# Optimization experiments

Measured on AMD Instinct MI355X. Metric: run time of the kernel, lower is better.

## Reference

```python
import jax, jax.numpy as jnp
import numpy as np

B, S, D = 1, 2048, 512
H, KH, DH = 8, 2, 64
G = H // KH            # grouped queries per kv head
CBS = SBS = 32         # compress / selection block size (equal)
NSEL = 8               # num selected blocks
WIN = 128              # sliding window size
NC = S // CBS          # num compressed blocks
NF = S // SBS          # num fine blocks (S divisible by SBS)
CDIM = CBS * DH


def setup_inputs():
    key = jax.random.key(0)
    ks = jax.random.split(key, 12)
    r = lambda k, shape, s=0.02: jax.random.normal(k, shape, dtype=jnp.float32) * s
    return {
        "inp": jax.random.normal(ks[0], (B, S, D), dtype=jnp.float32),
        "norm_w": jnp.ones((D,), jnp.float32),
        "w_qkv": r(ks[1], (D, H * DH + 2 * KH * DH)),
        "mem_kv": r(ks[2], (2, KH, 1, DH)),
        "k_pos": r(ks[3], (KH, CBS, DH)),
        "v_pos": r(ks[4], (KH, CBS, DH)),
        "kc_w1": r(ks[5], (CDIM, CDIM)), "kc_b1": jnp.zeros((CDIM,), jnp.float32),
        "kc_w2": r(ks[6], (CDIM, DH)), "kc_b2": jnp.zeros((DH,), jnp.float32),
        "vc_w1": r(ks[7], (CDIM, CDIM)), "vc_b1": jnp.zeros((CDIM,), jnp.float32),
        "vc_w2": r(ks[8], (CDIM, DH)), "vc_b2": jnp.zeros((DH,), jnp.float32),
        "comb_w": r(ks[9], (D, 3 * H)),
        "comb_b": jnp.tile(jnp.array([-2.0, -2.0, 2.0], jnp.float32), H),
        "out_w": r(ks[10], (H * DH, D)),
    }


def _rope(x):  # x: [b, h, n, d]; interleaved rotary (rotary-embedding-torch style)
    d, n = x.shape[-1], x.shape[-2]
    inv = 1.0 / (10000.0 ** (jnp.arange(0, d, 2, dtype=jnp.float32) / d))
    fr = jnp.arange(n, dtype=jnp.float32)[:, None] * inv[None, :]  # [n, d/2]
    fr = jnp.repeat(fr, 2, axis=-1)                                 # [n, d]
    cos, sin = jnp.cos(fr), jnp.sin(fr)
    xp = x.reshape(*x.shape[:-1], d // 2, 2)
    xr = jnp.stack((-xp[..., 1], xp[..., 0]), axis=-1).reshape(x.shape)
    return x * cos + xr * sin


def _mlp(x, w1, b1, w2, b2):
    return jax.nn.relu(x @ w1 + b1) @ w2 + b2


def _forward(inp, norm_w, w_qkv, mem_kv, k_pos, v_pos, kc_w1, kc_b1, kc_w2, kc_b2,
             vc_w1, vc_b1, vc_w2, vc_b2, comb_w, comb_b, out_w):
    scale = DH ** -0.5
    NEG = -jnp.finfo(jnp.float32).max

    # RMSNorm
    x = inp * jax.lax.rsqrt(jnp.mean(inp * inp, -1, keepdims=True)
                            + jnp.finfo(jnp.float32).eps) * norm_w

    qkv = x @ w_qkv
    q, k, v = jnp.split(qkv, [H * DH, H * DH + KH * DH], axis=-1)
    q = q.reshape(B, S, H, DH).transpose(0, 2, 1, 3)    # b h n d
    k = k.reshape(B, S, KH, DH).transpose(0, 2, 1, 3)   # b kh n d
    v = v.reshape(B, S, KH, DH).transpose(0, 2, 1, 3)

    # --- 1. compressed attention (unrotated q/k) ---
    kb = k.reshape(B, KH, NC, CBS, DH) + k_pos[None, :, None]
    vb = v.reshape(B, KH, NC, CBS, DH) + v_pos[None, :, None]
    ck = _mlp(kb.reshape(B, KH, NC, CDIM), kc_w1, kc_b1, kc_w2, kc_b2)  # b kh nc d
    cv = _mlp(vb.reshape(B, KH, NC, CDIM), vc_w1, vc_b1, vc_w2, vc_b2)
    ck = jnp.concatenate((jnp.broadcast_to(mem_kv[0][None], (B, KH, 1, DH)), ck), axis=2)
    cv = jnp.concatenate((jnp.broadcast_to(mem_kv[1][None], (B, KH, 1, DH)), cv), axis=2)

    ck_pos = jnp.concatenate((jnp.array([-1]), (jnp.arange(NC) + 1) * CBS - 1))
    cmask = ck_pos[None, :] < jnp.arange(S)[:, None]     # [S, 1+NC]

    qg = q.reshape(B, KH, G, S, DH)
    csim = jnp.einsum('bhgid,bhjd->bhgij', qg, ck) * scale
    csim = jnp.where(cmask, csim, NEG)
    cattn = jax.nn.softmax(csim, axis=-1)
    c_out = jnp.einsum('bhgij,bhjd->bhgid', cattn, cv)   # b kh g n d

    # --- importance scores -> top-k block selection (shared across grouped queries) ---
    imp = csim[..., 1:].mean(axis=2)                     # b kh n nc
    imp = jnp.pad(imp, ((0, 0), (0, 0), (0, 0), (1, 0)), constant_values=-1e3)
    imp = jax.nn.softmax(imp, axis=-1)[..., 1:]
    sel_val, sel_idx = jax.lax.top_k(imp, NSEL)          # b kh n sel

    # --- rotary for fine + sliding branches ---
    qr, kr = _rope(q), _rope(k)

    # --- 2. fine (selected-block) attention ---
    own = jnp.broadcast_to((jnp.arange(S) // SBS)[None, None, :, None], (B, KH, S, 1))
    sel_idx = jnp.concatenate((sel_idx, own), axis=-1)   # b kh n (sel+1), own block appended

    bmask = jnp.broadcast_to((sel_val > 1e-10)[..., None], (B, KH, S, NSEL, SBS))
    tri = jnp.tril(jnp.ones((SBS, SBS), bool))
    diag = jnp.broadcast_to(jnp.tile(tri, (NF, 1))[None, None, :, None, :], (B, KH, S, 1, SBS))
    fmask = jnp.concatenate((bmask, diag), axis=-2).reshape(B, KH, 1, S, (NSEL + 1) * SBS)

    kfb = kr.reshape(B, KH, NF, SBS, DH)
    vfb = v.reshape(B, KH, NF, SBS, DH)
    gidx = sel_idx[..., None, None]                      # b kh n sel1 1 1
    fk = jnp.take_along_axis(kfb[:, :, None], gidx, axis=3).reshape(B, KH, S, (NSEL + 1) * SBS, DH)
    fv = jnp.take_along_axis(vfb[:, :, None], gidx, axis=3).reshape(B, KH, S, (NSEL + 1) * SBS, DH)

    fqg = qr.reshape(B, KH, G, S, DH)
    fsim = jnp.einsum('bhgid,bhijd->bhgij', fqg, fk) * scale
    fsim = jnp.where(fmask, fsim, NEG)
    fattn = jax.nn.softmax(fsim, axis=-1)
    f_out = jnp.einsum('bhgij,bhijd->bhgid', fattn, fv)  # b kh g n d

    diff = jnp.arange(S)[:, None] - jnp.arange(S)[None, :]
    smask = (diff >= 0) & (diff <= WIN)
    ssim = jnp.einsum('bhgid,bhjd->bhgij', fqg, kr) * scale
    ssim = jnp.where(smask, ssim, NEG)
    sattn = jax.nn.softmax(ssim, axis=-1)
    s_out = jnp.einsum('bhgij,bhjd->bhgid', sattn, v)    # b kh g n d

    # --- learned gating combine over [compressed, fine, sliding] ---
    gates = jax.nn.sigmoid(x @ comb_w + comb_b).reshape(B, S, H, 3)
    gates = gates.transpose(0, 2, 1, 3).reshape(B, KH, G, S, 3)
    out = gates[..., 0:1] * c_out + gates[..., 1:2] * f_out + gates[..., 2:3] * s_out
    out = out.reshape(B, H, S, DH).transpose(0, 2, 1, 3).reshape(B, S, H * DH)
    return out @ out_w


def reference(inp, norm_w, w_qkv, mem_kv, k_pos, v_pos, kc_w1, kc_b1, kc_w2, kc_b2,
              vc_w1, vc_b1, vc_w2, vc_b2, comb_w, comb_b, out_w):
    return _forward(inp, norm_w, w_qkv, mem_kv, k_pos, v_pos, kc_w1, kc_b1, kc_w2, kc_b2,
                    vc_w1, vc_b1, vc_w2, vc_b2, comb_w, comb_b, out_w)
```

## Files before the change

kernel.cpp:

```cpp
#include <hip/hip_runtime.h>
#include <hip/hip_bf16.h>
#include <math.h>

#define S 2048
#define D 512
#define H 8
#define KH 2
#define DH 64
#define G 4
#define CBS 32
#define NSEL 8
#define WIN 128
#define NC 64
#define CDIM 2048

typedef __attribute__((ext_vector_type(8))) short bf16x8_t;
typedef __attribute__((ext_vector_type(4))) float f32x4_t;
typedef __attribute__((ext_vector_type(2))) _Float16 half2v;

static __device__ __forceinline__ unsigned short f2bf(float f) {
    union { float f; unsigned int u; } v; v.f = f;
    unsigned int r = (v.u + 0x7FFFu + ((v.u >> 16) & 1u)) >> 16;
    return (unsigned short)r;
}
static __device__ __forceinline__ float bf2f(unsigned short h) {
    union { unsigned int u; float f; } v; v.u = ((unsigned int)h) << 16;
    return v.f;
}
static __device__ __forceinline__ float bflo(unsigned int u) {
    union { unsigned int u; float f; } v; v.u = u << 16; return v.f;
}
static __device__ __forceinline__ float bfhi(unsigned int u) {
    union { unsigned int u; float f; } v; v.u = u & 0xffff0000u; return v.f;
}
static __device__ __forceinline__ unsigned short f2h(float f) {
    union { _Float16 h; unsigned short s; } v; v.h = (_Float16)f; return v.s;
}
static __device__ __forceinline__ float h2f(unsigned short u) {
    union { unsigned short s; _Float16 h; } v; v.s = u; return (float)v.h;
}
static __device__ __forceinline__ float dot2f16(unsigned int a, unsigned int b, float c) {
    union { unsigned int u; half2v h; } A, B; A.u = a; B.u = b;
    return __builtin_amdgcn_fdot2(A.h, B.h, c, false);
}

__global__ __launch_bounds__(256) void k_rmsnorm(const float* __restrict__ inp,
                                                 const float* __restrict__ w,
                                                 unsigned short* __restrict__ xbf) {
    int s = blockIdx.x; int t = threadIdx.x;
    const float* row = inp + (size_t)s * D;
    float a = row[t], b = row[t + 256];
    float ss = a * a + b * b;
    for (int off = 32; off; off >>= 1) ss += __shfl_xor(ss, off);
    __shared__ float red[4];
    if ((t & 63) == 0) red[t >> 6] = ss;
    __syncthreads();
    float tot = red[0] + red[1] + red[2] + red[3];
    float inv = rsqrtf(tot / (float)D + 1.1920929e-07f);
    xbf[(size_t)s * D + t]       = f2bf(a * inv * w[t]);
    xbf[(size_t)s * D + t + 256] = f2bf(b * inv * w[t + 256]);
}

__global__ void k_rope_table(float* __restrict__ ct, float* __restrict__ st) {
    int idx = blockIdx.x * 256 + threadIdx.x;
    int s = idx >> 5, p = idx & 31;
    float inv = powf(10000.0f, -(float)p / 32.0f);
    float fr = (float)s * inv;
    ct[idx] = cosf(fr); st[idx] = sinf(fr);
}

__global__ __launch_bounds__(256) void k_gemm0(
    const unsigned short* __restrict__ A,
    const float* __restrict__ W,
    const float* __restrict__ k_pos, const float* __restrict__ v_pos,
    const float* __restrict__ ct, const float* __restrict__ st,
    unsigned short* __restrict__ q16,
    unsigned short* __restrict__ qr16, unsigned short* __restrict__ kr16,
    unsigned short* __restrict__ v16, unsigned short* __restrict__ kbvb)
{
    const int K = 512, N = 768;
    __shared__ __align__(16) unsigned short As[64][40];
    __shared__ __align__(16) unsigned short Bs[64][40];
    int t = threadIdx.x;
    int m0 = blockIdx.y * 64, n0 = blockIdx.x * 64;
    int wave = t >> 6, lane = t & 63;
    int mh = wave & 1, nh = wave >> 1;
    f32x4_t acc[2][2] = {};
    int ar = t >> 2, ac = (t & 3) * 8;
    int bk = t >> 3, bn = (t & 7) * 8;
    int arow_l = lane & 15, kcol = (lane >> 4) * 8;
    uint4 aReg = *(const uint4*)&A[(size_t)(m0 + ar) * K + ac];
    const float4* wr = (const float4*)&W[(size_t)bk * N + n0 + bn];
    float4 w0 = wr[0], w1 = wr[1];
    for (int k0 = 0; k0 < K; k0 += 32) {
        __syncthreads();
        *(uint4*)&As[ar][ac] = aReg;
        unsigned short bp[8];
        bp[0] = f2bf(w0.x); bp[1] = f2bf(w0.y); bp[2] = f2bf(w0.z); bp[3] = f2bf(w0.w);
        bp[4] = f2bf(w1.x); bp[5] = f2bf(w1.y); bp[6] = f2bf(w1.z); bp[7] = f2bf(w1.w);
        #pragma unroll
        for (int j = 0; j < 8; ++j) Bs[bn + j][bk] = bp[j];
        __syncthreads();
        if (k0 + 32 < K) {
            aReg = *(const uint4*)&A[(size_t)(m0 + ar) * K + k0 + 32 + ac];
            wr = (const float4*)&W[(size_t)(k0 + 32 + bk) * N + n0 + bn];
            w0 = wr[0]; w1 = wr[1];
        }
        bf16x8_t a0 = *(const bf16x8_t*)&As[mh * 32 + arow_l][kcol];
        bf16x8_t a1 = *(const bf16x8_t*)&As[mh * 32 + 16 + arow_l][kcol];
        bf16x8_t b0v = *(const bf16x8_t*)&Bs[nh * 32 + arow_l][kcol];
        bf16x8_t b1v = *(const bf16x8_t*)&Bs[nh * 32 + 16 + arow_l][kcol];
        acc[0][0] = __builtin_amdgcn_mfma_f32_16x16x32_bf16(a0, b0v, acc[0][0], 0, 0, 0);
        acc[0][1] = __builtin_amdgcn_mfma_f32_16x16x32_bf16(a0, b1v, acc[0][1], 0, 0, 0);
        acc[1][0] = __builtin_amdgcn_mfma_f32_16x16x32_bf16(a1, b0v, acc[1][0], 0, 0, 0);
        acc[1][1] = __builtin_amdgcn_mfma_f32_16x16x32_bf16(a1, b1v, acc[1][1], 0, 0, 0);
    }
    #pragma unroll
    for (int mi = 0; mi < 2; ++mi)
    #pragma unroll
    for (int ni = 0; ni < 2; ++ni)
    #pragma unroll
    for (int r = 0; r < 4; ++r) {
        int gm = m0 + mh * 32 + mi * 16 + (lane >> 4) * 4 + r;
        int gn = n0 + nh * 32 + ni * 16 + (lane & 15);
        float val = acc[mi][ni][r];
        float part = __shfl_xor(val, 1);
        if (gn < 512) {
            int hh = gn >> 6, d = gn & 63;
            size_t idx = ((size_t)hh * S + gm) * DH + d;
            q16[idx] = f2h(val);
            int p = d >> 1;
            float cc = ct[gm * 32 + p], sn = st[gm * 32 + p];
            float y = (d & 1) ? (val * cc + part * sn) : (val * cc - part * sn);
            qr16[idx] = f2h(y);
        } else if (gn < 640) {
            int gk = gn - 512, khh = gk >> 6, d = gk & 63;
            size_t idx = ((size_t)khh * S + gm) * DH + d;
            int p = d >> 1;
            float cc = ct[gm * 32 + p], sn = st[gm * 32 + p];
            float y = (d & 1) ? (val * cc + part * sn) : (val * cc - part * sn);
            kr16[idx] = f2h(y);
            int tt = gm & 31, nc2 = gm >> 5;
            kbvb[((size_t)(khh * 64 + nc2)) * 2048 + tt * 64 + d] =
                f2bf(val + k_pos[(khh * CBS + tt) * 64 + d]);
        } else {
            int gv = gn - 640, khh = gv >> 6, d = gv & 63;
            size_t idx = ((size_t)khh * S + gm) * DH + d;
            v16[idx] = f2bf(val);
            int tt = gm & 31, nc2 = gm >> 5;
            kbvb[((size_t)(128 + khh * 64 + nc2)) * 2048 + tt * 64 + d] =
                f2bf(val + v_pos[(khh * CBS + tt) * 64 + d]);
        }
    }
}

template<int MODE>
__global__ __launch_bounds__(256) void k_gemm(
    const unsigned short* __restrict__ A,
    const float* __restrict__ B0,
    int M, int N, int K,
    float* __restrict__ outC)
{
    __shared__ __align__(16) unsigned short As[64][40];
    __shared__ __align__(16) unsigned short Bs[64][40];
    int t = threadIdx.x;
    int m0 = blockIdx.y * 64, n0 = blockIdx.x * 64;
    const float* W = B0;
    int wave = t >> 6, lane = t & 63;
    int mh = wave & 1, nh = wave >> 1;
    f32x4_t acc[2][2] = {};
    int ar = t >> 2, ac = (t & 3) * 8;
    int bk = t >> 3, bn = (t & 7) * 8;
    int arow_l = lane & 15, kcol = (lane >> 4) * 8;
    uint4 aReg = *(const uint4*)&A[(size_t)(m0 + ar) * K + ac];
    const float4* wr = (const float4*)&W[(size_t)bk * N + n0 + bn];
    float4 w0 = wr[0], w1 = wr[1];
    for (int k0 = 0; k0 < K; k0 += 32) {
        __syncthreads();
        *(uint4*)&As[ar][ac] = aReg;
        unsigned short bp[8];
        bp[0] = f2bf(w0.x); bp[1] = f2bf(w0.y); bp[2] = f2bf(w0.z); bp[3] = f2bf(w0.w);
        bp[4] = f2bf(w1.x); bp[5] = f2bf(w1.y); bp[6] = f2bf(w1.z); bp[7] = f2bf(w1.w);
        #pragma unroll
        for (int j = 0; j < 8; ++j) Bs[bn + j][bk] = bp[j];
        __syncthreads();
        if (k0 + 32 < K) {
            aReg = *(const uint4*)&A[(size_t)(m0 + ar) * K + k0 + 32 + ac];
            wr = (const float4*)&W[(size_t)(k0 + 32 + bk) * N + n0 + bn];
            w0 = wr[0]; w1 = wr[1];
        }
        bf16x8_t a0 = *(const bf16x8_t*)&As[mh * 32 + arow_l][kcol];
        bf16x8_t a1 = *(const bf16x8_t*)&As[mh * 32 + 16 + arow_l][kcol];
        bf16x8_t b0v = *(const bf16x8_t*)&Bs[nh * 32 + arow_l][kcol];
        bf16x8_t b1v = *(const bf16x8_t*)&Bs[nh * 32 + 16 + arow_l][kcol];
        acc[0][0] = __builtin_amdgcn_mfma_f32_16x16x32_bf16(a0, b0v, acc[0][0], 0, 0, 0);
        acc[0][1] = __builtin_amdgcn_mfma_f32_16x16x32_bf16(a0, b1v, acc[0][1], 0, 0, 0);
        acc[1][0] = __builtin_amdgcn_mfma_f32_16x16x32_bf16(a1, b0v, acc[1][0], 0, 0, 0);
        acc[1][1] = __builtin_amdgcn_mfma_f32_16x16x32_bf16(a1, b1v, acc[1][1], 0, 0, 0);
    }
    #pragma unroll
    for (int mi = 0; mi < 2; ++mi)
    #pragma unroll
    for (int ni = 0; ni < 2; ++ni)
    #pragma unroll
    for (int r = 0; r < 4; ++r) {
        int gm = m0 + mh * 32 + mi * 16 + (lane >> 4) * 4 + r;
        int gn = n0 + nh * 32 + ni * 16 + (lane & 15);
        outC[(size_t)gm * N + gn] = acc[mi][ni][r];
    }
}

__global__ __launch_bounds__(256) void k_gemm1p(
    const unsigned short* __restrict__ A,
    const float* __restrict__ kc_w1, const float* __restrict__ vc_w1,
    float* __restrict__ part)
{
    const int N = 2048, LDA = 2048;
    __shared__ __align__(16) unsigned short As[64][40];
    __shared__ __align__(16) unsigned short Bs[64][40];
    int t = threadIdx.x;
    int mb = blockIdx.y & 3, ks = blockIdx.y >> 2;
    int m0 = mb * 64, n0 = blockIdx.x * 64, kbeg = ks * 1024;
    const float* W = (mb >= 2) ? vc_w1 : kc_w1;
    int wave = t >> 6, lane = t & 63;
    int mh = wave & 1, nh = wave >> 1;
    f32x4_t acc[2][2] = {};
    int ar = t >> 2, ac = (t & 3) * 8;
    int bk = t >> 3, bn = (t & 7) * 8;
    int arow_l = lane & 15, kcol = (lane >> 4) * 8;
    uint4 aReg = *(const uint4*)&A[(size_t)(m0 + ar) * LDA + kbeg + ac];
    const float4* wr = (const float4*)&W[(size_t)(kbeg + bk) * N + n0 + bn];
    float4 w0 = wr[0], w1 = wr[1];
    for (int k0 = 0; k0 < 1024; k0 += 32) {
        __syncthreads();
        *(uint4*)&As[ar][ac] = aReg;
        unsigned short bp[8];
        bp[0] = f2bf(w0.x); bp[1] = f2bf(w0.y); bp[2] = f2bf(w0.z); bp[3] = f2bf(w0.w);
        bp[4] = f2bf(w1.x); bp[5] = f2bf(w1.y); bp[6] = f2bf(w1.z); bp[7] = f2bf(w1.w);
        #pragma unroll
        for (int j = 0; j < 8; ++j) Bs[bn + j][bk] = bp[j];
        __syncthreads();
        if (k0 + 32 < 1024) {
            aReg = *(const uint4*)&A[(size_t)(m0 + ar) * LDA + kbeg + k0 + 32 + ac];
            wr = (const float4*)&W[(size_t)(kbeg + k0 + 32 + bk) * N + n0 + bn];
            w0 = wr[0]; w1 = wr[1];
        }
        bf16x8_t a0 = *(const bf16x8_t*)&As[mh * 32 + arow_l][kcol];
        bf16x8_t a1 = *(const bf16x8_t*)&As[mh * 32 + 16 + arow_l][kcol];
        bf16x8_t b0v = *(const bf16x8_t*)&Bs[nh * 32 + arow_l][kcol];
        bf16x8_t b1v = *(const bf16x8_t*)&Bs[nh * 32 + 16 + arow_l][kcol];
        acc[0][0] = __builtin_amdgcn_mfma_f32_16x16x32_bf16(a0, b0v, acc[0][0], 0, 0, 0);
        acc[0][1] = __builtin_amdgcn_mfma_f32_16x16x32_bf16(a0, b1v, acc[0][1], 0, 0, 0);
        acc[1][0] = __builtin_amdgcn_mfma_f32_16x16x32_bf16(a1, b0v, acc[1][0], 0, 0, 0);
        acc[1][1] = __builtin_amdgcn_mfma_f32_16x16x32_bf16(a1, b1v, acc[1][1], 0, 0, 0);
    }
    #pragma unroll
    for (int mi = 0; mi < 2; ++mi)
    #pragma unroll
    for (int ni = 0; ni < 2; ++ni)
    #pragma unroll
    for (int r = 0; r < 4; ++r) {
        int gm = m0 + mh * 32 + mi * 16 + (lane >> 4) * 4 + r;
        int gn = n0 + nh * 32 + ni * 16 + (lane & 15);
        part[((size_t)ks * 256 + gm) * N + gn] = acc[mi][ni][r];
    }
}

__global__ __launch_bounds__(256) void k_gemm1r(
    const float4* __restrict__ part, const float* __restrict__ kc_b1,
    const float* __restrict__ vc_b1, uint2* __restrict__ hid)
{
    int idx = blockIdx.x * 256 + threadIdx.x;
    int gm = idx >> 9, gn4 = (idx & 511) * 4;
    float4 a = part[idx], b = part[idx + 131072];
    const float* bias = (gm >= 128) ? vc_b1 : kc_b1;
    float r0 = fmaxf(a.x + b.x + bias[gn4 + 0], 0.f);
    float r1 = fmaxf(a.y + b.y + bias[gn4 + 1], 0.f);
    float r2 = fmaxf(a.z + b.z + bias[gn4 + 2], 0.f);
    float r3 = fmaxf(a.w + b.w + bias[gn4 + 3], 0.f);
    uint2 o;
    o.x = (unsigned)f2bf(r0) | ((unsigned)f2bf(r1) << 16);
    o.y = (unsigned)f2bf(r2) | ((unsigned)f2bf(r3) << 16);
    hid[idx] = o;
}

__global__ __launch_bounds__(256) void k_mlp2p(
    const unsigned short* __restrict__ A,
    const float* __restrict__ kc_w2, const float* __restrict__ vc_w2,
    float* __restrict__ part)
{
    const int N = 64, LDA = 2048;
    __shared__ __align__(16) unsigned short As[64][40];
    __shared__ __align__(16) unsigned short Bs[64][40];
    int t = threadIdx.x;
    int ks = blockIdx.x, m0 = blockIdx.y * 64;
    int kbeg = ks * 512;
    const float* W = (blockIdx.y >= 2) ? vc_w2 : kc_w2;
    int wave = t >> 6, lane = t & 63;
    int mh = wave & 1, nh = wave >> 1;
    f32x4_t acc[2][2] = {};
    int ar = t >> 2, ac = (t & 3) * 8;
    int bk = t >> 3, bn = (t & 7) * 8;
    int arow_l = lane & 15, kcol = (lane >> 4) * 8;
    uint4 aReg = *(const uint4*)&A[(size_t)(m0 + ar) * LDA + kbeg + ac];
    const float4* wr = (const float4*)&W[(size_t)(kbeg + bk) * N + bn];
    float4 w0 = wr[0], w1 = wr[1];
    for (int k0 = 0; k0 < 512; k0 += 32) {
        __syncthreads();
        *(uint4*)&As[ar][ac] = aReg;
        unsigned short bp[8];
        bp[0] = f2bf(w0.x); bp[1] = f2bf(w0.y); bp[2] = f2bf(w0.z); bp[3] = f2bf(w0.w);
        bp[4] = f2bf(w1.x); bp[5] = f2bf(w1.y); bp[6] = f2bf(w1.z); bp[7] = f2bf(w1.w);
        #pragma unroll
        for (int j = 0; j < 8; ++j) Bs[bn + j][bk] = bp[j];
        __syncthreads();
        if (k0 + 32 < 512) {
            aReg = *(const uint4*)&A[(size_t)(m0 + ar) * LDA + kbeg + k0 + 32 + ac];
            wr = (const float4*)&W[(size_t)(kbeg + k0 + 32 + bk) * N + bn];
            w0 = wr[0]; w1 = wr[1];
        }
        bf16x8_t a0 = *(const bf16x8_t*)&As[mh * 32 + arow_l][kcol];
        bf16x8_t a1 = *(const bf16x8_t*)&As[mh * 32 + 16 + arow_l][kcol];
        bf16x8_t b0v = *(const bf16x8_t*)&Bs[nh * 32 + arow_l][kcol];
        bf16x8_t b1v = *(const bf16x8_t*)&Bs[nh * 32 + 16 + arow_l][kcol];
        acc[0][0] = __builtin_amdgcn_mfma_f32_16x16x32_bf16(a0, b0v, acc[0][0], 0, 0, 0);
        acc[0][1] = __builtin_amdgcn_mfma_f32_16x16x32_bf16(a0, b1v, acc[0][1], 0, 0, 0);
        acc[1][0] = __builtin_amdgcn_mfma_f32_16x16x32_bf16(a1, b0v, acc[1][0], 0, 0, 0);
        acc[1][1] = __builtin_amdgcn_mfma_f32_16x16x32_bf16(a1, b1v, acc[1][1], 0, 0, 0);
    }
    #pragma unroll
    for (int mi = 0; mi < 2; ++mi)
    #pragma unroll
    for (int ni = 0; ni < 2; ++ni)
    #pragma unroll
    for (int r = 0; r < 4; ++r) {
        int gm = m0 + mh * 32 + mi * 16 + (lane >> 4) * 4 + r;
        int gn = nh * 32 + ni * 16 + (lane & 15);
        part[((size_t)ks * 256 + gm) * 64 + gn] = acc[mi][ni][r];
    }
}

__global__ __launch_bounds__(256) void k_mlp2r(
    const float* __restrict__ part, const float* __restrict__ kc_b2,
    const float* __restrict__ vc_b2, const float* __restrict__ mem_kv,
    unsigned short* __restrict__ ck16, float* __restrict__ cv)
{
    int idx = blockIdx.x * 256 + threadIdx.x;
    int gm = idx >> 6, gn = idx & 63;
    float sum = part[(size_t)gm * 64 + gn] + part[(size_t)(256 + gm) * 64 + gn]
              + part[(size_t)(512 + gm) * 64 + gn] + part[(size_t)(768 + gm) * 64 + gn];
    bool isv = gm >= 128;
    sum += isv ? vc_b2[gn] : kc_b2[gn];
    int kh2 = (gm >> 6) & 1, nc2 = gm & 63;
    if (isv) cv[(kh2 * 65 + 1 + nc2) * 64 + gn] = sum;
    else     ck16[(kh2 * 65 + 1 + nc2) * 64 + gn] = f2h(sum);
    if (blockIdx.x == 0 && threadIdx.x < 256) {
        int t = threadIdx.x;
        int path2 = t >> 7, khm = (t >> 6) & 1, dm = t & 63;
        float mv = mem_kv[path2 * (KH * DH) + khm * DH + dm];
        if (path2) cv[khm * 65 * 64 + dm] = mv;
        else       ck16[khm * 65 * 64 + dm] = f2h(mv);
    }
}

__global__ __launch_bounds__(256) void k_cattn(
    const unsigned short* __restrict__ q16, const unsigned short* __restrict__ ck16,
    const float* __restrict__ cv,
    float* __restrict__ c_out, int* __restrict__ sel)
{
    int kh = blockIdx.x >> 9, sc = blockIdx.x & 511;
    int s_base = sc * 4;
    __shared__ __align__(16) unsigned char KL[64 * 128];
    __shared__ float cvL[64][66];
    __shared__ unsigned short qL16[4][64];
    __shared__ float simL[4][64];
    __shared__ float pL[4][64];
    int t = threadIdx.x;
    {
        int j = t >> 2, gp = (t & 3) * 2;
        const uint4* src = (const uint4*)&ck16[((size_t)kh * 65 + j) * 64];
        uint4 a = src[gp], b = src[gp + 1];
        *(uint4*)(KL + j * 128 + 16 * (gp ^ (j & 7)))       = a;
        *(uint4*)(KL + j * 128 + 16 * ((gp + 1) ^ (j & 7))) = b;
    }
    for (int idx = t; idx < 4096; idx += 256) {
        int j = idx >> 6, d = idx & 63;
        cvL[j][d] = cv[(kh * 65 + j) * 64 + d];
    }
    int g = t >> 6, lane = t & 63;
    for (int si = 0; si < 4; ++si) {
        int s = s_base + si;
        __syncthreads();
        qL16[g][lane] = q16[((kh * G + g) * S + s) * DH + lane];
        __syncthreads();
        int j = lane;
        bool valid = (j == 0) || (s >= j * 32);
        float sva = 0.f, svb = 0.f, svc = 0.f, svd = 0.f;
        #pragma unroll
        for (int grp = 0; grp < 8; ++grp) {
            uint4 kk = *(const uint4*)(KL + j * 128 + 16 * (grp ^ (j & 7)));
            uint4 qq = *(const uint4*)((const unsigned char*)qL16 + g * 128 + 16 * grp);
            sva = dot2f16(kk.x, qq.x, sva);
            svb = dot2f16(kk.y, qq.y, svb);
            svc = dot2f16(kk.z, qq.z, svc);
            svd = dot2f16(kk.w, qq.w, svd);
        }
        float sim = ((sva + svb) + (svc + svd)) * 0.125f;
        float simm = valid ? sim : -INFINITY;
        simL[g][j] = simm;
        float m = simm;
        for (int off = 32; off; off >>= 1) m = fmaxf(m, __shfl_xor(m, off));
        float p = valid ? __expf(simm - m) : 0.f;
        float den = p;
        for (int off = 32; off; off >>= 1) den += __shfl_xor(den, off);
        pL[g][j] = p / den;
        float acc = 0.f;
        #pragma unroll
        for (int j4 = 0; j4 < 16; ++j4) {
            float4 p4 = *(const float4*)&pL[g][j4 * 4];
            acc += p4.x * cvL[j4 * 4 + 0][lane] + p4.y * cvL[j4 * 4 + 1][lane]
                 + p4.z * cvL[j4 * 4 + 2][lane] + p4.w * cvL[j4 * 4 + 3][lane];
        }
        c_out[((kh * G + g) * S + s) * DH + lane] = acc;
        __syncthreads();
        if (g == 0) {
            int l = lane;
            float lv = -INFINITY;
            if (l < 63 && s >= (l + 1) * 32)
                lv = 0.25f * (simL[0][l + 1] + simL[1][l + 1] + simL[2][l + 1] + simL[3][l + 1]);
            float mm = lv;
            for (int off = 32; off; off >>= 1) mm = fmaxf(mm, __shfl_xor(mm, off));
            mm = fmaxf(mm, -1000.0f);
            float e = (lv == -INFINITY) ? 0.f : __expf(lv - mm);
            float dd = e;
            for (int off = 32; off; off >>= 1) dd += __shfl_xor(dd, off);
            dd += __expf(-1000.0f - mm);
            float val = e / dd;
            float vc = val;
            int base = (kh * S + s) * 9;
            for (int t8 = 0; t8 < 8; ++t8) {
                float bv2 = vc; int bi = l;
                for (int off = 32; off; off >>= 1) {
                    float ov = __shfl_xor(bv2, off); int oi = __shfl_xor(bi, off);
                    if (ov > bv2 || (ov == bv2 && oi < bi)) { bv2 = ov; bi = oi; }
                }
                if (l == 0) sel[base + t8] = (bv2 > 1e-10f) ? bi : -1;
                if (l == bi) vc = -1.f;
            }
            if (l == 0) sel[base + 8] = s >> 5;
        }
    }
}

__global__ __launch_bounds__(256, 4) void k_swattn(
    const unsigned short* __restrict__ qr16, const unsigned short* __restrict__ kr16,
    const unsigned short* __restrict__ v16, const int* __restrict__ sel,
    float* __restrict__ fob, float* __restrict__ sob)
{
    int kh = blockIdx.x >> 11, s = blockIdx.x & 2047;
    int t = threadIdx.x, w = t >> 6, lane = t & 63, g = w;
    __shared__ __align__(16) unsigned char KL[64 * 128];
    __shared__ __align__(16) unsigned char VL[64 * 144];
    __shared__ unsigned short qL16[4][64];
    __shared__ float pL[4][64];

    qL16[g][lane] = qr16[(((size_t)kh * G + g) * S + s) * DH + lane];

    int base = (kh * S + s) * 9;
    int lo = s - WIN; if (lo < 0) lo = 0;

    int nv = 0;
    #pragma unroll
    for (int i = 0; i < 8; ++i) nv += (sel[base + i] >= 0) ? 1 : 0;
    int npairF = (nv + 1) >> 1;
    int nchS = (s - lo + 63) >> 6;
    int nch = npairF + nchS;
    int ownStart = s & ~31;
    bool hasOwn = (s & 31) != 0;

    float lF = 0.f, lS = 0.f;
    float a0F = 0.f, a1F = 0.f, a0S = 0.f, a1S = 0.f;
    int h = lane >> 5, dhalf = lane & 31;
    int key = w * 16 + (lane & 15);
    int grpA = lane >> 4;
    uint4 z = make_uint4(0, 0, 0, 0);
    uint4 kd0 = z, kd1 = z, vd0 = z, vd1 = z;

    auto issue = [&](int c) {
        int gkey; bool kv;
        if (c < npairF) {
            int b = sel[base + 2 * c + ((key >> 5) & 1)];
            kv = b >= 0;
            gkey = (kv ? b : 0) * 32 + (key & 31);
        } else {
            gkey = lo + (c - npairF) * 64 + key;
            kv = gkey < s;
        }
        const uint4* kp = (const uint4*)&kr16[((size_t)kh * S + gkey) * DH];
        const uint4* vp = (const uint4*)&v16 [((size_t)kh * S + gkey) * DH];
        kd0 = kv ? kp[grpA] : z;
        kd1 = kv ? kp[grpA + 4] : z;
        vd0 = kv ? vp[grpA] : z;
        vd1 = kv ? vp[grpA + 4] : z;
    };

    issue(0);
    for (int c = 0; c < nch; ++c) {
        __syncthreads();
        *(uint4*)(KL + key * 128 + 16 * (grpA ^ (key & 7))) = kd0;
        *(uint4*)(KL + key * 128 + 16 * ((grpA + 4) ^ (key & 7))) = kd1;
        *(uint4*)(VL + key * 144 + 16 * grpA) = vd0;
        *(uint4*)(VL + key * 144 + 16 * (grpA + 4)) = vd1;
        __syncthreads();
        if (c + 1 < nch) issue(c + 1);

        int j = lane;
        bool isPair = c < npairF;
        int cs = c - npairF;
        int gk0 = lo + cs * 64;
        bool valid = isPair ? ((j < 32) || ((2 * c + 1) < nv))
                            : ((gk0 + j) < s);

        float sva = 0.f, svb = 0.f, svc = 0.f, svd = 0.f;
        #pragma unroll
        for (int grp = 0; grp < 8; ++grp) {
            uint4 kk = *(const uint4*)(KL + j * 128 + 16 * (grp ^ (j & 7)));
            uint4 qq = *(const uint4*)((const unsigned char*)qL16 + g * 128 + 16 * grp);
            sva = dot2f16(kk.x, qq.x, sva);
            svb = dot2f16(kk.y, qq.y, svb);
            svc = dot2f16(kk.z, qq.z, svc);
            svd = dot2f16(kk.w, qq.w, svd);
        }
        float sv = (sva + svb) + (svc + svd);
        float p = valid ? __expf(sv * 0.125f) : 0.f;
        pL[g][j] = p;

        bool doOwn = (!isPair) && hasOwn && (cs == nchS - 1);
        if (!doOwn) {
            if (isPair) lF += p; else lS += p;
            float t0 = 0.f, t1 = 0.f;
            #pragma unroll
            for (int j4 = 0; j4 < 8; ++j4) {
                float4 p4 = *(const float4*)&pL[g][h * 32 + j4 * 4];
                const float* pp = (const float*)&p4;
                #pragma unroll
                for (int q2 = 0; q2 < 4; ++q2) {
                    unsigned int v2 = *(const unsigned int*)(VL + (h * 32 + j4 * 4 + q2) * 144 + 4 * dhalf);
                    t0 += pp[q2] * bflo(v2);
                    t1 += pp[q2] * bfhi(v2);
                }
            }
            if (isPair) { a0F += t0; a1F += t1; }
            else        { a0S += t0; a1S += t1; }
        } else {
            lS += p;
            int jstart = ownStart - gk0;
            if (j >= jstart) lF += p;
            float pre0 = 0.f, pre1 = 0.f, suf0 = 0.f, suf1 = 0.f;
            #pragma unroll
            for (int j4 = 0; j4 < 8; ++j4) {
                float4 p4 = *(const float4*)&pL[g][h * 32 + j4 * 4];
                const float* pp = (const float*)&p4;
                #pragma unroll
                for (int q2 = 0; q2 < 4; ++q2) {
                    int jj = h * 32 + j4 * 4 + q2;
                    unsigned int v2 = *(const unsigned int*)(VL + jj * 144 + 4 * dhalf);
                    float t0 = pp[q2] * bflo(v2);
                    float t1 = pp[q2] * bfhi(v2);
                    bool inSuf = jj >= jstart;
                    suf0 += inSuf ? t0 : 0.f;
                    suf1 += inSuf ? t1 : 0.f;
                    pre0 += inSuf ? 0.f : t0;
                    pre1 += inSuf ? 0.f : t1;
                }
            }
            a0S += pre0 + suf0; a1S += pre1 + suf1;
            a0F += suf0;        a1F += suf1;
        }
    }
    {
        float pr = h2f(qL16[g][lane]) * h2f(kr16[((size_t)kh * S + s) * DH + lane]);
        for (int off = 32; off; off >>= 1) pr += __shfl_xor(pr, off);
        float pd = __expf(pr * 0.125f);
        for (int off = 32; off; off >>= 1) {
            lF += __shfl_xor(lF, off);
            lS += __shfl_xor(lS, off);
        }
        lF += pd; lS += pd;
        if (h == 0) {
            unsigned int v2 = *(const unsigned int*)&v16[(((size_t)kh * S + s) * DH) + 2 * dhalf];
            float b0 = bflo(v2), b1 = bfhi(v2);
            a0F += pd * b0; a1F += pd * b1;
            a0S += pd * b0; a1S += pd * b1;
        }
    }
    a0F += __shfl_xor(a0F, 32);
    a1F += __shfl_xor(a1F, 32);
    a0S += __shfl_xor(a0S, 32);
    a1S += __shfl_xor(a1S, 32);
    if (lane < 32) {
        size_t ob = (((size_t)kh * G + g) * S + s) * DH + 2 * dhalf;
        float invF = 1.f / lF, invS = 1.f / lS;
        *(float2*)&fob[ob] = make_float2(a0F * invF, a1F * invF);
        *(float2*)&sob[ob] = make_float2(a0S * invS, a1S * invS);
    }
}

__global__ __launch_bounds__(256) void k_combine(
    const unsigned short* __restrict__ xbf, const float* __restrict__ comb_w, const float* __restrict__ comb_b,
    const float* __restrict__ c_out, const float* __restrict__ f_out, const float* __restrict__ s_out,
    unsigned short* __restrict__ comb)
{
    int s = blockIdx.x, t = threadIdx.x;
    __shared__ float gpart[24][8];
    __shared__ float gates[24];
    if (t < 192) {
        int cc = t >> 3, pt = t & 7;
        float sum = 0.f;
        for (int d = pt * 64; d < pt * 64 + 64; ++d)
            sum += bf2f(xbf[s * D + d]) * comb_w[d * 24 + cc];
        gpart[cc][pt] = sum;
    }
    __syncthreads();
    if (t < 24) {
        float sum = comb_b[t];
        for (int i = 0; i < 8; ++i) sum += gpart[t][i];
        gates[t] = 1.f / (1.f + __expf(-sum));
    }
    __syncthreads();
    for (int o = t; o < 512; o += 256) {
        int h = o >> 6, d = o & 63;
        int idx = (h * S + s) * DH + d;
        float r = gates[h * 3] * c_out[idx] + gates[h * 3 + 1] * f_out[idx] + gates[h * 3 + 2] * s_out[idx];
        comb[s * D + o] = f2bf(r);
    }
}

extern "C" void kernel_launch(void* const* d_in, const int* in_sizes, int n_in,
                              void* d_out, int out_size, void* d_ws, size_t ws_size,
                              hipStream_t stream)
{
    (void)in_sizes; (void)n_in; (void)out_size; (void)ws_size;
    const float* inp    = (const float*)d_in[0];
    const float* norm_w = (const float*)d_in[1];
    const float* w_qkv  = (const float*)d_in[2];
    const float* mem_kv = (const float*)d_in[3];
    const float* k_pos  = (const float*)d_in[4];
    const float* v_pos  = (const float*)d_in[5];
    const float* kc_w1  = (const float*)d_in[6];
    const float* kc_b1  = (const float*)d_in[7];
    const float* kc_w2  = (const float*)d_in[8];
    const float* kc_b2  = (const float*)d_in[9];
    const float* vc_w1  = (const float*)d_in[10];
    const float* vc_b1  = (const float*)d_in[11];
    const float* vc_w2  = (const float*)d_in[12];
    const float* vc_b2  = (const float*)d_in[13];
    const float* comb_w = (const float*)d_in[14];
    const float* comb_b = (const float*)d_in[15];
    const float* out_w  = (const float*)d_in[16];
    float* out = (float*)d_out;

    char* w = (char*)d_ws;
    size_t off = 0;
    auto alloc = [&](size_t bytes) { void* p = w + off; off += (bytes + 255) & ~(size_t)255; return p; };
    unsigned short* xbf   = (unsigned short*)alloc((size_t)S * D * 2);
    unsigned short* kbvb  = (unsigned short*)alloc((size_t)256 * 2048 * 2);
    unsigned short* hid   = (unsigned short*)alloc((size_t)256 * 2048 * 2);
    unsigned short* combb = (unsigned short*)alloc((size_t)S * 512 * 2);
    unsigned short* q16   = (unsigned short*)alloc((size_t)H * S * DH * 2);
    unsigned short* qr16  = (unsigned short*)alloc((size_t)H * S * DH * 2);
    unsigned short* kr16  = (unsigned short*)alloc((size_t)KH * S * DH * 2);
    unsigned short* v16   = (unsigned short*)alloc((size_t)KH * S * DH * 2);
    unsigned short* ck16  = (unsigned short*)alloc((size_t)KH * 65 * 64 * 2);
    float* cvb  = (float*)alloc((size_t)KH * 65 * 64 * 4);
    float* cob  = (float*)alloc((size_t)H * S * DH * 4);
    float* fob  = (float*)alloc((size_t)H * S * DH * 4);
    float* sob  = (float*)alloc((size_t)H * S * DH * 4);
    float* ctab = (float*)alloc((size_t)S * 32 * 4);
    float* stab = (float*)alloc((size_t)S * 32 * 4);
    float* partb = (float*)alloc((size_t)4 * 256 * 64 * 4);
    float* g1part = (float*)alloc((size_t)2 * 256 * 2048 * 4);
    int*   selb = (int*)alloc((size_t)KH * S * 9 * 4);

    k_rope_table<<<(S * 32) / 256, 256, 0, stream>>>(ctab, stab);

    k_rmsnorm<<<S, 256, 0, stream>>>(inp, norm_w, xbf);

    k_gemm0<<<dim3(768 / 64, S / 64), 256, 0, stream>>>(
        xbf, w_qkv, k_pos, v_pos, ctab, stab, q16, qr16, kr16, v16, kbvb);

    k_gemm1p<<<dim3(32, 8), 256, 0, stream>>>(kbvb, kc_w1, vc_w1, g1part);
    k_gemm1r<<<512, 256, 0, stream>>>((const float4*)g1part, kc_b1, vc_b1, (uint2*)hid);

    k_mlp2p<<<dim3(4, 4), 256, 0, stream>>>(hid, kc_w2, vc_w2, partb);
    k_mlp2r<<<64, 256, 0, stream>>>(partb, kc_b2, vc_b2, mem_kv, ck16, cvb);

    k_cattn<<<KH * 512, 256, 0, stream>>>(q16, ck16, cvb, cob, selb);

    k_swattn<<<KH * S, 256, 0, stream>>>(qr16, kr16, v16, selb, fob, sob);

    k_combine<<<S, 256, 0, stream>>>(xbf, comb_w, comb_b, cob, fob, sob, combb);
    k_gemm<2><<<dim3(512 / 64, S / 64), 256, 0, stream>>>(
        combb, out_w, S, 512, 512, out);
}
```

Before: 218.3 us.

## Double-buffer K/V tiles in sliding attention, hold q in registers, fuse prep kernels

The sliding/fine attention kernel now uses two LDS buffers for K/V tiles. The next chunk is staged while the current one is consumed, which cuts the loop from two barriers per chunk to one. The query vector is kept in registers instead of LDS. The RMSNorm and rope-table kernels are merged into a single launch to save one launch. In exchange, LDS use roughly doubles and register pressure rises, which may lower occupancy under launch_bounds(256,4).

New measurement: 213.7 us. -2.1%, faster.

```diff
diff --git a/kernel.cpp b/kernel.cpp
--- a/kernel.cpp
+++ b/kernel.cpp
@@ -44,29 +44,30 @@
     return __builtin_amdgcn_fdot2(A.h, B.h, c, false);
 }
 
-__global__ __launch_bounds__(256) void k_rmsnorm(const float* __restrict__ inp,
-                                                 const float* __restrict__ w,
-                                                 unsigned short* __restrict__ xbf) {
-    int s = blockIdx.x; int t = threadIdx.x;
-    const float* row = inp + (size_t)s * D;
-    float a = row[t], b = row[t + 256];
-    float ss = a * a + b * b;
-    for (int off = 32; off; off >>= 1) ss += __shfl_xor(ss, off);
-    __shared__ float red[4];
-    if ((t & 63) == 0) red[t >> 6] = ss;
-    __syncthreads();
-    float tot = red[0] + red[1] + red[2] + red[3];
-    float inv = rsqrtf(tot / (float)D + 1.1920929e-07f);
-    xbf[(size_t)s * D + t]       = f2bf(a * inv * w[t]);
-    xbf[(size_t)s * D + t + 256] = f2bf(b * inv * w[t + 256]);
-}
-
-__global__ void k_rope_table(float* __restrict__ ct, float* __restrict__ st) {
-    int idx = blockIdx.x * 256 + threadIdx.x;
-    int s = idx >> 5, p = idx & 31;
-    float inv = powf(10000.0f, -(float)p / 32.0f);
-    float fr = (float)s * inv;
-    ct[idx] = cosf(fr); st[idx] = sinf(fr);
+__global__ __launch_bounds__(256) void k_prep(const float* __restrict__ inp,
+                                              const float* __restrict__ w,
+                                              unsigned short* __restrict__ xbf,
+                                              float* __restrict__ ct, float* __restrict__ st) {
+    int b = blockIdx.x, t = threadIdx.x;
+    if (b < S) {
+        const float* row = inp + (size_t)b * D;
+        float a = row[t], c = row[t + 256];
+        float ss = a * a + c * c;
+        for (int off = 32; off; off >>= 1) ss += __shfl_xor(ss, off);
+        __shared__ float red[4];
+        if ((t & 63) == 0) red[t >> 6] = ss;
+        __syncthreads();
+        float tot = red[0] + red[1] + red[2] + red[3];
+        float inv = rsqrtf(tot / (float)D + 1.1920929e-07f);
+        xbf[(size_t)b * D + t]       = f2bf(a * inv * w[t]);
+        xbf[(size_t)b * D + t + 256] = f2bf(c * inv * w[t + 256]);
+    } else {
+        int idx = (b - S) * 256 + t;
+        int s = idx >> 5, p = idx & 31;
+        float inv = powf(10000.0f, -(float)p / 32.0f);
+        float fr = (float)s * inv;
+        ct[idx] = cosf(fr); st[idx] = sinf(fr);
+    }
 }
 
 __global__ __launch_bounds__(256) void k_gemm0(
@@ -459,12 +460,13 @@
 {
     int kh = blockIdx.x >> 11, s = blockIdx.x & 2047;
     int t = threadIdx.x, w = t >> 6, lane = t & 63, g = w;
-    __shared__ __align__(16) unsigned char KL[64 * 128];
-    __shared__ __align__(16) unsigned char VL[64 * 144];
-    __shared__ unsigned short qL16[4][64];
+    __shared__ __align__(16) unsigned char KL[2][64 * 128];
+    __shared__ __align__(16) unsigned char VL[2][64 * 144];
     __shared__ float pL[4][64];
 
-    qL16[g][lane] = qr16[(((size_t)kh * G + g) * S + s) * DH + lane];
+    const uint4* qp = (const uint4*)&qr16[(((size_t)kh * G + g) * S + s) * DH];
+    uint4 qq0 = qp[0], qq1 = qp[1], qq2 = qp[2], qq3 = qp[3];
+    uint4 qq4 = qp[4], qq5 = qp[5], qq6 = qp[6], qq7 = qp[7];
 
     int base = (kh * S + s) * 9;
     int lo = s - WIN; if (lo < 0) lo = 0;
@@ -503,16 +505,21 @@
         vd0 = kv ? vp[grpA] : z;
         vd1 = kv ? vp[grpA + 4] : z;
     };
+    auto stage = [&](int buf) {
+        *(uint4*)(KL[buf] + key * 128 + 16 * (grpA ^ (key & 7))) = kd0;
+        *(uint4*)(KL[buf] + key * 128 + 16 * ((grpA + 4) ^ (key & 7))) = kd1;
+        *(uint4*)(VL[buf] + key * 144 + 16 * grpA) = vd0;
+        *(uint4*)(VL[buf] + key * 144 + 16 * (grpA + 4)) = vd1;
+    };
 
     issue(0);
+    stage(0);
+    if (nch > 1) issue(1);
+    __syncthreads();
+
     for (int c = 0; c < nch; ++c) {
-        __syncthreads();
-        *(uint4*)(KL + key * 128 + 16 * (grpA ^ (key & 7))) = kd0;
-        *(uint4*)(KL + key * 128 + 16 * ((grpA + 4) ^ (key & 7))) = kd1;
-        *(uint4*)(VL + key * 144 + 16 * grpA) = vd0;
-        *(uint4*)(VL + key * 144 + 16 * (grpA + 4)) = vd1;
-        __syncthreads();
-        if (c + 1 < nch) issue(c + 1);
+        const unsigned char* KLc = KL[c & 1];
+        const unsigned char* VLc = VL[c & 1];
 
         int j = lane;
         bool isPair = c < npairF;
@@ -522,15 +529,13 @@
                             : ((gk0 + j) < s);
 
         float sva = 0.f, svb = 0.f, svc = 0.f, svd = 0.f;
-        #pragma unroll
-        for (int grp = 0; grp < 8; ++grp) {
-            uint4 kk = *(const uint4*)(KL + j * 128 + 16 * (grp ^ (j & 7)));
-            uint4 qq = *(const uint4*)((const unsigned char*)qL16 + g * 128 + 16 * grp);
-            sva = dot2f16(kk.x, qq.x, sva);
-            svb = dot2f16(kk.y, qq.y, svb);
-            svc = dot2f16(kk.z, qq.z, svc);
-            svd = dot2f16(kk.w, qq.w, svd);
-        }
+        #define QKSTEP(G_, QQ_) { \
+            uint4 kk = *(const uint4*)(KLc + j * 128 + 16 * ((G_) ^ (j & 7))); \
+            sva = dot2f16(kk.x, QQ_.x, sva); svb = dot2f16(kk.y, QQ_.y, svb); \
+            svc = dot2f16(kk.z, QQ_.z, svc); svd = dot2f16(kk.w, QQ_.w, svd); }
+        QKSTEP(0, qq0) QKSTEP(1, qq1) QKSTEP(2, qq2) QKSTEP(3, qq3)
+        QKSTEP(4, qq4) QKSTEP(5, qq5) QKSTEP(6, qq6) QKSTEP(7, qq7)
+        #undef QKSTEP
         float sv = (sva + svb) + (svc + svd);
         float p = valid ? __expf(sv * 0.125f) : 0.f;
         pL[g][j] = p;
@@ -545,7 +550,7 @@
                 const float* pp = (const float*)&p4;
                 #pragma unroll
                 for (int q2 = 0; q2 < 4; ++q2) {
-                    unsigned int v2 = *(const unsigned int*)(VL + (h * 32 + j4 * 4 + q2) * 144 + 4 * dhalf);
+                    unsigned int v2 = *(const unsigned int*)(VLc + (h * 32 + j4 * 4 + q2) * 144 + 4 * dhalf);
                     t0 += pp[q2] * bflo(v2);
                     t1 += pp[q2] * bfhi(v2);
                 }
@@ -564,7 +569,7 @@
                 #pragma unroll
                 for (int q2 = 0; q2 < 4; ++q2) {
                     int jj = h * 32 + j4 * 4 + q2;
-                    unsigned int v2 = *(const unsigned int*)(VL + jj * 144 + 4 * dhalf);
+                    unsigned int v2 = *(const unsigned int*)(VLc + jj * 144 + 4 * dhalf);
                     float t0 = pp[q2] * bflo(v2);
                     float t1 = pp[q2] * bfhi(v2);
                     bool inSuf = jj >= jstart;
@@ -577,9 +582,16 @@
             a0S += pre0 + suf0; a1S += pre1 + suf1;
             a0F += suf0;        a1F += suf1;
         }
+
+        if (c + 1 < nch) {
+            stage((c + 1) & 1);
+            if (c + 2 < nch) issue(c + 2);
+        }
+        __syncthreads();
     }
     {
-        float pr = h2f(qL16[g][lane]) * h2f(kr16[((size_t)kh * S + s) * DH + lane]);
+        float qd = h2f(qr16[(((size_t)kh * G + g) * S + s) * DH + lane]);
+        float pr = qd * h2f(kr16[((size_t)kh * S + s) * DH + lane]);
         for (int off = 32; off; off >>= 1) pr += __shfl_xor(pr, off);
         float pd = __expf(pr * 0.125f);
         for (int off = 32; off; off >>= 1) {
@@ -682,9 +694,7 @@
     float* g1part = (float*)alloc((size_t)2 * 256 * 2048 * 4);
     int*   selb = (int*)alloc((size_t)KH * S * 9 * 4);
 
-    k_rope_table<<<(S * 32) / 256, 256, 0, stream>>>(ctab, stab);
-
-    k_rmsnorm<<<S, 256, 0, stream>>>(inp, norm_w, xbf);
+    k_prep<<<S + 256, 256, 0, stream>>>(inp, norm_w, xbf, ctab, stab);
 
     k_gemm0<<<dim3(768 / 64, S / 64), 256, 0, stream>>>(
         xbf, w_qkv, k_pos, v_pos, ctab, stab, q16, qr16, kr16, v16, kbvb);
```
